# Optimization experiments

Measured on AMD Instinct MI355X. Metric: run time of the kernel, lower is better.

Reference implementation:

```python
import jax, jax.numpy as jnp
import numpy as np

N = 50000
IN_DIM = 128
HEADS = 4
HEAD_DIM = IN_DIM // HEADS
TYPE_NUM = 3
E = 800000
NEG_SLOPE = 0.2


def setup_inputs() -> dict:
    key = jax.random.key(0)
    k1, k2, k3, k4, k5 = jax.random.split(key, 5)
    embedding = jax.random.normal(k1, (N, IN_DIM), dtype=jnp.float32)
    edges = jax.random.randint(k2, (TYPE_NUM, 2, E), 0, N, dtype=jnp.int32)
    W = jax.random.normal(k3, (TYPE_NUM, IN_DIM, HEADS, HEAD_DIM), dtype=jnp.float32) * 0.05
    a_src = jax.random.normal(k4, (TYPE_NUM, HEADS, HEAD_DIM), dtype=jnp.float32) * 0.05
    a_dst = jax.random.normal(k5, (TYPE_NUM, HEADS, HEAD_DIM), dtype=jnp.float32) * 0.05
    return {"embedding": embedding, "edges": edges, "W": W, "a_src": a_src, "a_dst": a_dst}


def _gat_layer(x, ei, W_t, asrc_t, adst_t):
    # x: [N, IN_DIM]; ei: [2, E]; W_t: [IN_DIM, H, D]
    h = jnp.einsum('nd,dhk->nhk', x, W_t)                  # [N, H, D]
    e_src = jnp.sum(h * asrc_t, axis=-1)                   # [N, H]
    e_dst = jnp.sum(h * adst_t, axis=-1)                   # [N, H]
    src, dst = ei[0], ei[1]
    e = jax.nn.leaky_relu(e_src[src] + e_dst[dst], NEG_SLOPE)  # [E, H]
    m = jax.ops.segment_max(e, dst, num_segments=N)        # [N, H]
    e = jnp.exp(e - m[dst])
    denom = jax.ops.segment_sum(e, dst, num_segments=N)    # [N, H]
    msg = h[src] * e[:, :, None]                           # [E, H, D]
    agg = jax.ops.segment_sum(msg, dst, num_segments=N)    # [N, H, D]
    out = agg / (denom[:, :, None] + 1e-9)
    return jax.nn.elu(out.reshape(N, HEADS * HEAD_DIM))


def reference(embedding, edges, W, a_src, a_dst):
    features_gat = [_gat_layer(embedding, edges[i], W[i], a_src[i], a_dst[i])
                    for i in range(TYPE_NUM)]
    # NOTE: the original module (faithfully) also uses the GAT layers for the
    # 'gcn' branch: features_gcn = [self.gat_layers[i](...) for ...]
    features_gcn = [_gat_layer(embedding, edges[i], W[i], a_src[i], a_dst[i])
                    for i in range(TYPE_NUM)]
    return (jnp.stack(features_gat), jnp.stack(features_gcn))
```

## Files before the change

### kernel.cpp

```cpp
#include <hip/hip_runtime.h>
#include <hip/hip_fp16.h>
#include <math.h>

#define NN 50000
#define IND 128
#define NH 4
#define NE 800000
#define NT 3
#define NSLOPE 0.2f

#define TILE 48
#define NBPT 1042
#define NBTOT (NT * NBPT)
#define BCAP 960

#define SCB ((NT * NE + 8191) / 8192)
#define GXB ((NN + 127) / 128)

typedef _Float16 f16x8 __attribute__((ext_vector_type(8)));
typedef float    f32x4 __attribute__((ext_vector_type(4)));

__device__ __forceinline__ unsigned pk_add_f16(unsigned a, unsigned b) {
    __half2 x = *reinterpret_cast<__half2*>(&a);
    __half2 y = *reinterpret_cast<__half2*>(&b);
    __half2 r = __hadd2(x, y);
    return *reinterpret_cast<unsigned*>(&r);
}

__global__ __launch_bounds__(256) void prep_kernel(
    const float* __restrict__ W, __half* __restrict__ wt16g, int* __restrict__ gcursor)
{
    int idx = blockIdx.x * 256 + threadIdx.x;
    if (idx < NT * IND * IND) {
        int t = idx / (IND * IND), r = idx - t * (IND * IND);
        int k = r >> 7, c = r & 127;
        wt16g[((size_t)t * IND + c) * IND + k] = (__half)W[idx];
    }
    if (idx < NBTOT) gcursor[idx] = idx * BCAP;
}

__global__ __launch_bounds__(512) void scatter_gemm_kernel(
    const int* __restrict__ edges, int* __restrict__ gcursor, unsigned* __restrict__ bucketed,
    const float* __restrict__ x, const __half* __restrict__ wt16g,
    const float* __restrict__ asrc, const float* __restrict__ adst,
    __half* __restrict__ h16, float* __restrict__ es, float* __restrict__ ed)
{
    __shared__ __align__(16) char ldsbuf[34816];
    const int tid = threadIdx.x;

    if (blockIdx.x < SCB) {
        int* cnt = (int*)ldsbuf;
        int* bas = cnt + NBTOT;
        for (int i = tid; i < NBTOT; i += 512) cnt[i] = 0;
        __syncthreads();
        const long long gtot = (long long)NT * NE;
        const long long g0 = (long long)blockIdx.x * 8192;
        long long g1 = g0 + 8192; if (g1 > gtot) g1 = gtot;
        for (long long g = g0 + tid; g < g1; g += 512) {
            int t = (g >= 2LL * NE) ? 2 : (g >= NE ? 1 : 0);
            int e = (int)(g - (long long)t * NE);
            int d = edges[(size_t)t * 2 * NE + NE + e];
            atomicAdd(&cnt[t * NBPT + d / TILE], 1);
        }
        __syncthreads();
        for (int i = tid; i < NBTOT; i += 512) {
            int c = cnt[i];
            bas[i] = c ? atomicAdd(&gcursor[i], c) : 0;
            cnt[i] = 0;
        }
        __syncthreads();
        for (long long g = g0 + tid; g < g1; g += 512) {
            int t = (g >= 2LL * NE) ? 2 : (g >= NE ? 1 : 0);
            int e = (int)(g - (long long)t * NE);
            const int* eb = edges + (size_t)t * 2 * NE;
            int s = eb[e], d = eb[NE + e];
            int bkt = d / TILE;
            int bg = t * NBPT + bkt;
            int pos = bas[bg] + atomicAdd(&cnt[bg], 1);
            bucketed[pos] = (unsigned)s | ((unsigned)(d - bkt * TILE) << 16);
        }
        return;
    }

    const int bx = blockIdx.x - SCB;
    const int t  = bx / GXB;
    const int gx = bx - t * GXB;
    __half* tile = (__half*)ldsbuf;
    const int wid = tid >> 6, lane = tid & 63;
    __half* tl = tile + wid * (16 * 136);
    const int l15 = lane & 15, l4 = lane >> 4;
    const int r0 = gx * 128 + wid * 16;
    if (r0 >= NN) return;

    const __half* wt = wt16g + (size_t)t * IND * IND;
    const float* xrow = x + (size_t)(r0 + l15) * IND;

    f32x4 acc[8];
    #pragma unroll
    for (int i = 0; i < 8; i++) acc[i] = (f32x4){0.f, 0.f, 0.f, 0.f};

    #pragma unroll
    for (int ks = 0; ks < 4; ks++) {
        const int kb = ks * 32 + l4 * 8;
        float4 x0 = *reinterpret_cast<const float4*>(xrow + kb);
        float4 x1 = *reinterpret_cast<const float4*>(xrow + kb + 4);
        f16x8 af;
        af[0] = (_Float16)x0.x; af[1] = (_Float16)x0.y;
        af[2] = (_Float16)x0.z; af[3] = (_Float16)x0.w;
        af[4] = (_Float16)x1.x; af[5] = (_Float16)x1.y;
        af[6] = (_Float16)x1.z; af[7] = (_Float16)x1.w;
        #pragma unroll
        for (int ct = 0; ct < 8; ct++) {
            f16x8 bf = *reinterpret_cast<const f16x8*>(wt + (size_t)(ct * 16 + l15) * IND + kb);
            acc[ct] = __builtin_amdgcn_mfma_f32_16x16x32_f16(af, bf, acc[ct], 0, 0, 0);
        }
    }

    #pragma unroll
    for (int ct = 0; ct < 8; ct++)
        #pragma unroll
        for (int r = 0; r < 4; r++)
            tl[(l4 * 4 + r) * 136 + ct * 16 + l15] = (__half)acc[ct][r];
    __syncthreads();

    {
        #pragma unroll
        for (int i = 0; i < 4; i++) {
            int c = lane + 64 * i;
            int row = c >> 4, off = (c & 15) * 8;
            f16x8 v = *reinterpret_cast<const f16x8*>(tl + row * 136 + off);
            *reinterpret_cast<f16x8*>(h16 + ((size_t)t * NN + r0 + row) * IND + off) = v;
        }
        int row16 = lane >> 2, head = lane & 3;
        const __half* hr = tl + row16 * 136 + head * 32;
        const float* av = asrc + ((size_t)t * NH + head) * 32;
        const float* bv = adst + ((size_t)t * NH + head) * 32;
        float se = 0.f, de = 0.f;
        #pragma unroll
        for (int jj = 0; jj < 4; jj++) {
            f16x8 hv = *reinterpret_cast<const f16x8*>(hr + jj * 8);
            #pragma unroll
            for (int j = 0; j < 8; j++) {
                float hf = (float)hv[j];
                se = fmaf(hf, av[jj * 8 + j], se);
                de = fmaf(hf, bv[jj * 8 + j], de);
            }
        }
        int n = r0 + row16;
        es[((size_t)t * NN + n) * NH + head] = se;
        ed[((size_t)t * NN + n) * NH + head] = de;
    }
}

__global__ __launch_bounds__(512) void gat_bucket_kernel(
    const unsigned* __restrict__ bucketed, const int* __restrict__ gcursor,
    const float* __restrict__ es, const float* __restrict__ ed,
    const __half* __restrict__ h16, float* __restrict__ out)
{
    __shared__ unsigned pk[BCAP];
    __shared__ unsigned srt[BCAP];
    __shared__ int hist[64], scn[64], cur[64];
    const int bg = blockIdx.x;
    const int t = bg / NBPT;
    const int node0 = (bg - t * NBPT) * TILE;
    const int tid = threadIdx.x;
    const int base = bg * BCAP;
    const int cnt = gcursor[bg] - base;

    if (tid < 64) { hist[tid] = 0; cur[tid] = 0; }
    __syncthreads();
    for (int i = tid; i < cnt; i += 512) {
        unsigned v = __builtin_nontemporal_load(&bucketed[base + i]);
        pk[i] = v;
        atomicAdd(&hist[(v >> 16) & 63u], 1);
    }
    __syncthreads();
    if (tid < 64) {
        int v = hist[tid];
        int inc = v;
        #pragma unroll
        for (int off = 1; off < 64; off <<= 1) {
            int n = __shfl_up(inc, off, 64);
            if (tid >= off) inc += n;
        }
        scn[tid] = inc - v;
    }
    __syncthreads();
    for (int i = tid; i < cnt; i += 512) {
        unsigned v = pk[i];
        int dl = (int)((v >> 16) & 63u);
        int pos = scn[dl] + atomicAdd(&cur[dl], 1);
        srt[pos] = v & 0xFFFFu;
    }
    __syncthreads();

    const int wid = tid >> 6, lane = tid & 63;
    const int el2 = lane >> 4;
    const int dl3 = lane & 15;
    const int hsel = dl3 >> 2;
    const float* es_t = es + (size_t)t * NN * NH;
    const __half* h16_t = h16 + (size_t)t * NN * IND;

    for (int j = 0; j < 6; j++) {
        const int dloc = wid * 6 + j;
        const int node = node0 + dloc;
        if (node >= NN) break;
        const int beg = scn[dloc], nE = hist[dloc];
        const float edv = ed[((size_t)t * NN + node) * NH + (lane & 3)];

        unsigned p0 = 0u, p1 = 0u, p2 = 0u, p3 = 0u;
        float dsum = 0.f;

        for (int b2 = 0; b2 < nE; b2 += 16) {
            int ne = nE - b2; if (ne > 16) ne = 16;
            const int ei = lane >> 2;
            float wv = 0.f; int sv = 0; unsigned wpk = 0u;
            if (ei < ne) {
                sv = (int)srt[beg + b2 + ei];
                float s = es_t[(sv << 2) + (lane & 3)] + edv;
                s = s > 0.f ? s : NSLOPE * s;
                wv = __expf(s);
                dsum += wv;
                __half2 w2 = __float2half2_rn(wv);
                wpk = *reinterpret_cast<unsigned*>(&w2);
            }
            for (int kk = 0; kk < ne; kk += 4) {
                int sl = (kk + el2) << 2;
                int      sb = __shfl(sv, sl, 64);
                unsigned wb = (unsigned)__shfl((int)wpk, sl | hsel, 64);
                if (kk + el2 < ne) {
                    uint4 hv = *reinterpret_cast<const uint4*>(h16_t + ((size_t)sb << 7) + (dl3 << 3));
                    asm("v_pk_fma_f16 %0, %1, %2, %0" : "+v"(p0) : "v"(hv.x), "v"(wb));
                    asm("v_pk_fma_f16 %0, %1, %2, %0" : "+v"(p1) : "v"(hv.y), "v"(wb));
                    asm("v_pk_fma_f16 %0, %1, %2, %0" : "+v"(p2) : "v"(hv.z), "v"(wb));
                    asm("v_pk_fma_f16 %0, %1, %2, %0" : "+v"(p3) : "v"(hv.w), "v"(wb));
                }
            }
        }

        #pragma unroll
        for (int m = 4; m <= 32; m <<= 1) dsum += __shfl_xor(dsum, m, 64);
        #pragma unroll
        for (int m = 16; m <= 32; m <<= 1) {
            p0 = pk_add_f16(p0, (unsigned)__shfl_xor((int)p0, m, 64));
            p1 = pk_add_f16(p1, (unsigned)__shfl_xor((int)p1, m, 64));
            p2 = pk_add_f16(p2, (unsigned)__shfl_xor((int)p2, m, 64));
            p3 = pk_add_f16(p3, (unsigned)__shfl_xor((int)p3, m, 64));
        }
        float dn = __shfl(dsum, hsel, 64) + 1e-9f;

        if (el2 == 0) {
            float rn = 1.f / dn;
            float2 f0 = __half22float2(*reinterpret_cast<__half2*>(&p0));
            float2 f1 = __half22float2(*reinterpret_cast<__half2*>(&p1));
            float2 f2 = __half22float2(*reinterpret_cast<__half2*>(&p2));
            float2 f3 = __half22float2(*reinterpret_cast<__half2*>(&p3));
            float v0=f0.x*rn, v1=f0.y*rn, v2=f1.x*rn, v3=f1.y*rn;
            float v4=f2.x*rn, v5=f2.y*rn, v6=f3.x*rn, v7=f3.y*rn;
            f32x4 o0, o1;
            o0[0] = v0 > 0.f ? v0 : expm1f(v0);
            o0[1] = v1 > 0.f ? v1 : expm1f(v1);
            o0[2] = v2 > 0.f ? v2 : expm1f(v2);
            o0[3] = v3 > 0.f ? v3 : expm1f(v3);
            o1[0] = v4 > 0.f ? v4 : expm1f(v4);
            o1[1] = v5 > 0.f ? v5 : expm1f(v5);
            o1[2] = v6 > 0.f ? v6 : expm1f(v6);
            o1[3] = v7 > 0.f ? v7 : expm1f(v7);
            float* obase = out + (size_t)t * NN * IND + ((size_t)node << 7) + (dl3 << 3);
            float* obase2 = obase + (size_t)NT * NN * IND;
            __builtin_nontemporal_store(o0, reinterpret_cast<f32x4*>(obase));
            __builtin_nontemporal_store(o1, reinterpret_cast<f32x4*>(obase + 4));
            __builtin_nontemporal_store(o0, reinterpret_cast<f32x4*>(obase2));
            __builtin_nontemporal_store(o1, reinterpret_cast<f32x4*>(obase2 + 4));
        }
    }
}

extern "C" void kernel_launch(void* const* d_in, const int* in_sizes, int n_in,
                              void* d_out, int out_size, void* d_ws, size_t ws_size,
                              hipStream_t stream)
{
    const float* x     = (const float*)d_in[0];
    const int*   edges = (const int*)d_in[1];
    const float* W     = (const float*)d_in[2];
    const float* asrc  = (const float*)d_in[3];
    const float* adst  = (const float*)d_in[4];
    float* out = (float*)d_out;

    char* p = (char*)d_ws;
    __half*   h16      = (__half*)p;   p += (size_t)NT * NN * IND * 2;
    float*    es       = (float*)p;    p += (size_t)NT * NN * NH * 4;
    float*    ed       = (float*)p;    p += (size_t)NT * NN * NH * 4;
    int*      gcursor  = (int*)p;      p += (size_t)NBTOT * 4;
    __half*   wt16g    = (__half*)p;   p += (size_t)NT * IND * IND * 2;
    unsigned* bucketed = (unsigned*)p; p += ((size_t)NBTOT * BCAP + 1024) * 4;

    prep_kernel<<<(NT * IND * IND + 255) / 256, 256, 0, stream>>>(W, wt16g, gcursor);
    scatter_gemm_kernel<<<SCB + NT * GXB, 512, 0, stream>>>(
        edges, gcursor, bucketed, x, wt16g, asrc, adst, h16, es, ed);
    gat_bucket_kernel<<<NBTOT, 512, 0, stream>>>(bucketed, gcursor, es, ed, h16, out);
}
```

Before: 202.2 us.

## Pad per-node edge lists to multiples of four and enlarge scatter chunks

Each destination node's sorted edge segment is padded up to a multiple of four with dummy entries that carry zero weight and point at node zero. This drops the per-iteration bounds check around the gather and FMA in the inner loop, so the loop runs without divergence. The scatter phase also processes 32768 edges per block instead of 8192, which means fewer blocks and fewer global cursor atomics, but less parallelism in that phase. Padding adds some wasted gathers of row zero.

After: 217.0 us. +7.4%, slower.

```diff
diff --git a/kernel.cpp b/kernel.cpp
--- a/kernel.cpp
+++ b/kernel.cpp
@@ -13,8 +13,11 @@
 #define NBPT 1042
 #define NBTOT (NT * NBPT)
 #define BCAP 960
-
-#define SCB ((NT * NE + 8191) / 8192)
+#define SRTCAP (BCAP + 3 * TILE)
+#define DUMMY 0xFFFFu
+
+#define SEB 32768
+#define SCB ((NT * NE + SEB - 1) / SEB)
 #define GXB ((NN + 127) / 128)
 
 typedef _Float16 f16x8 __attribute__((ext_vector_type(8)));
@@ -54,8 +57,8 @@
         for (int i = tid; i < NBTOT; i += 512) cnt[i] = 0;
         __syncthreads();
         const long long gtot = (long long)NT * NE;
-        const long long g0 = (long long)blockIdx.x * 8192;
-        long long g1 = g0 + 8192; if (g1 > gtot) g1 = gtot;
+        const long long g0 = (long long)blockIdx.x * SEB;
+        long long g1 = g0 + SEB; if (g1 > gtot) g1 = gtot;
         for (long long g = g0 + tid; g < g1; g += 512) {
             int t = (g >= 2LL * NE) ? 2 : (g >= NE ? 1 : 0);
             int e = (int)(g - (long long)t * NE);
@@ -158,7 +161,7 @@
     const __half* __restrict__ h16, float* __restrict__ out)
 {
     __shared__ unsigned pk[BCAP];
-    __shared__ unsigned srt[BCAP];
+    __shared__ unsigned srt[SRTCAP];
     __shared__ int hist[64], scn[64], cur[64];
     const int bg = blockIdx.x;
     const int t = bg / NBPT;
@@ -177,13 +180,14 @@
     __syncthreads();
     if (tid < 64) {
         int v = hist[tid];
-        int inc = v;
+        int v4 = (v + 3) & ~3;
+        int inc = v4;
         #pragma unroll
         for (int off = 1; off < 64; off <<= 1) {
             int n = __shfl_up(inc, off, 64);
             if (tid >= off) inc += n;
         }
-        scn[tid] = inc - v;
+        scn[tid] = inc - v4;
     }
     __syncthreads();
     for (int i = tid; i < cnt; i += 512) {
@@ -191,6 +195,10 @@
         int dl = (int)((v >> 16) & 63u);
         int pos = scn[dl] + atomicAdd(&cur[dl], 1);
         srt[pos] = v & 0xFFFFu;
+    }
+    if (tid < 64) {
+        int h = hist[tid], h4 = (h + 3) & ~3, b = scn[tid];
+        for (int i = h; i < h4; i++) srt[b + i] = DUMMY;
     }
     __syncthreads();
 
@@ -205,7 +213,8 @@
         const int dloc = wid * 6 + j;
         const int node = node0 + dloc;
         if (node >= NN) break;
-        const int beg = scn[dloc], nE = hist[dloc];
+        const int beg = scn[dloc];
+        const int nE = (hist[dloc] + 3) & ~3;
         const float edv = ed[((size_t)t * NN + node) * NH + (lane & 3)];
 
         unsigned p0 = 0u, p1 = 0u, p2 = 0u, p3 = 0u;
@@ -214,27 +223,28 @@
         for (int b2 = 0; b2 < nE; b2 += 16) {
             int ne = nE - b2; if (ne > 16) ne = 16;
             const int ei = lane >> 2;
-            float wv = 0.f; int sv = 0; unsigned wpk = 0u;
+            int sv = 0; unsigned wpk = 0u;
             if (ei < ne) {
-                sv = (int)srt[beg + b2 + ei];
-                float s = es_t[(sv << 2) + (lane & 3)] + edv;
-                s = s > 0.f ? s : NSLOPE * s;
-                wv = __expf(s);
-                dsum += wv;
-                __half2 w2 = __float2half2_rn(wv);
-                wpk = *reinterpret_cast<unsigned*>(&w2);
+                unsigned svr = srt[beg + b2 + ei];
+                if (svr != DUMMY) {
+                    float s = es_t[(svr << 2) + (lane & 3)] + edv;
+                    s = s > 0.f ? s : NSLOPE * s;
+                    float wv = __expf(s);
+                    dsum += wv;
+                    __half2 w2 = __float2half2_rn(wv);
+                    wpk = *reinterpret_cast<unsigned*>(&w2);
+                    sv = (int)svr;
+                }
             }
             for (int kk = 0; kk < ne; kk += 4) {
                 int sl = (kk + el2) << 2;
                 int      sb = __shfl(sv, sl, 64);
                 unsigned wb = (unsigned)__shfl((int)wpk, sl | hsel, 64);
-                if (kk + el2 < ne) {
-                    uint4 hv = *reinterpret_cast<const uint4*>(h16_t + ((size_t)sb << 7) + (dl3 << 3));
-                    asm("v_pk_fma_f16 %0, %1, %2, %0" : "+v"(p0) : "v"(hv.x), "v"(wb));
-                    asm("v_pk_fma_f16 %0, %1, %2, %0" : "+v"(p1) : "v"(hv.y), "v"(wb));
-                    asm("v_pk_fma_f16 %0, %1, %2, %0" : "+v"(p2) : "v"(hv.z), "v"(wb));
-                    asm("v_pk_fma_f16 %0, %1, %2, %0" : "+v"(p3) : "v"(hv.w), "v"(wb));
-                }
+                uint4 hv = *reinterpret_cast<const uint4*>(h16_t + ((size_t)sb << 7) + (dl3 << 3));
+                asm("v_pk_fma_f16 %0, %1, %2, %0" : "+v"(p0) : "v"(hv.x), "v"(wb));
+                asm("v_pk_fma_f16 %0, %1, %2, %0" : "+v"(p1) : "v"(hv.y), "v"(wb));
+                asm("v_pk_fma_f16 %0, %1, %2, %0" : "+v"(p2) : "v"(hv.z), "v"(wb));
+                asm("v_pk_fma_f16 %0, %1, %2, %0" : "+v"(p3) : "v"(hv.w), "v"(wb));
             }
         }
 
```
